# Performance work log

Measured on AMD Instinct MI355X. Metric: run time of the kernel, lower is better.

## Reference

```python
import jax, jax.numpy as jnp
import numpy as np
import math

STRIDES = (8, 16, 32, 64, 128)
IMAGE_SIZE = 1024
NUM_CLASSES = 81
B, N = 8, 64


def _calc_level_thresholds(strides, image_size):
    result = []
    last_size = image_size
    for i in range(len(strides) - 1, -1, -1):
        s = strides[i]
        pixel_size = float(s) / image_size
        th_max = math.ceil(last_size / s)
        if th_max % 2:
            th_max += 1
        th_min = th_max // 2
        last_size = th_min * s
        if i == 0:
            th_min = 1
        result.append((th_min * pixel_size, th_max * pixel_size))
    return tuple(result[::-1])


LEVEL_TH = _calc_level_thresholds(STRIDES, IMAGE_SIZE)


def setup_inputs():
    key = jax.random.key(0)
    kb, kl = jax.random.split(key)
    # normalized xyxy boxes with x1<x2, y1<y2
    xy = jax.random.uniform(kb, (B, N, 2, 2), dtype=jnp.float32)
    mins = jnp.min(xy, axis=2)
    maxs = jnp.clip(jnp.max(xy, axis=2) + 0.01, 0.0, 1.0)
    boxes = jnp.concatenate([mins, maxs], axis=-1)  # (B, N, 4)
    labels = jax.random.randint(kl, (B, N), 1, NUM_CLASSES)  # foreground classes (0 = background)
    return {"boxes": boxes, "labels": labels}


def _map_level(boxes, labels, stride, th):
    # boxes sorted by descending area along axis 1, so the LAST matching box
    Bn, Nn = boxes.shape[:2]
    H = IMAGE_SIZE // stride
    ps = stride / IMAGE_SIZE
    coords = (jnp.arange(H, dtype=boxes.dtype) + 0.5) * ps  # normalized cell centers
    mx = coords[None, None, None, :]  # varies along W
    my = coords[None, None, :, None]  # varies along H
    x1 = boxes[..., 0][:, :, None, None]
    y1 = boxes[..., 1][:, :, None, None]
    x2 = boxes[..., 2][:, :, None, None]
    y2 = boxes[..., 3][:, :, None, None]
    l = mx - x1
    t = my - y1
    r = x2 - mx
    b = y2 - my  # (B, N, H, W)
    mn = jnp.minimum(jnp.minimum(l, t), jnp.minimum(r, b))
    mxv = jnp.maximum(jnp.maximum(l, t), jnp.maximum(r, b))
    fg = mn >= 0                                   # inside-box mask (_filter_background)
    pred = fg & (mxv > th[0]) & (mxv <= th[1])     # level fit (_pointwise_fit_in_level)
    box_idx = jnp.arange(Nn)[None, :, None, None]
    win = jnp.max(jnp.where(pred, box_idx, -1), axis=1)
    has_win = win >= 0
    winc = jnp.maximum(win, 0)
    bidx = jnp.arange(Bn)[:, None, None]
    bw = boxes[bidx, winc]   # (B, H, W, 4) winning box per cell
    lw = labels[bidx, winc]  # (B, H, W)
    gx = coords[None, None, :]
    gy = coords[None, :, None]
    lL = gx - bw[..., 0]
    tT = gy - bw[..., 1]
    rR = bw[..., 2] - gx
    bB = bw[..., 3] - gy
    reg = jnp.where(has_win[..., None], jnp.stack([lL, tT, rR, bB], axis=-1), 0.0)
    dx = jnp.minimum(lL, rR)
    Dx = jnp.maximum(lL, rR)
    dy = jnp.minimum(tT, bB)
    Dy = jnp.maximum(tT, bB)
    arg = (dx / jnp.where(Dx != 0, Dx, 1.0)) * (dy / jnp.where(Dy != 0, Dy, 1.0))
    cent = jnp.where(has_win & (arg > 0), jnp.sqrt(jnp.where(arg > 0, arg, 1.0)), 0.0)
    # class map: winner one-hot; otherwise background channel 1 unless any box covers the cell
    fg_any = jnp.any(fg, axis=1)  # (B, H, W) -- _clear_box_background accumulated effect
    onehot = jax.nn.one_hot(lw, NUM_CLASSES, dtype=boxes.dtype)
    bg = jnp.zeros_like(onehot).at[..., 0].set(jnp.where(fg_any, 0.0, 1.0))
    cls = jnp.where(has_win[..., None], onehot, bg)
    level_map = jnp.concatenate([reg, cent[..., None], cls], axis=-1)  # (B, H, W, 5+C)
    return jnp.transpose(level_map, (0, 3, 1, 2))  # (B, 5+C, H, W)


def _forward(boxes, labels):
    area = (boxes[..., 2] - boxes[..., 0]) * (boxes[..., 3] - boxes[..., 1])
    order = jnp.argsort(-area, axis=1)  # descending area, as in sorted(..., reverse=True)
    boxes_s = jnp.take_along_axis(boxes, order[..., None], axis=1)
    labels_s = jnp.take_along_axis(labels, order, axis=1)
    return tuple(_map_level(boxes_s, labels_s, s, th) for s, th in zip(STRIDES, LEVEL_TH))


def reference(boxes, labels):
    return _forward(boxes, labels)
```

## Files before the change

kernel.cpp:

```cpp
#include <hip/hip_runtime.h>

#define NBATCH 8
#define NBOX   64
#define NCLS   81
#define NCH    86


__global__ __launch_bounds__(64) void fcos_mapper(
    const float* __restrict__ boxes,
    const int*   __restrict__ labels,
    float*       __restrict__ out)
{
    const int tid = threadIdx.x;
    const int bid = blockIdx.x;

    int rel, logH; float ps, tlo, thi; int base0;
    if (bid < 2048)      { rel = bid;        logH = 7; ps = 0.0078125f; tlo = 0.0078125f; thi = 0.0625f; base0 = 0; }
    else if (bid < 2560) { rel = bid - 2048; logH = 6; ps = 0.015625f;  tlo = 0.0625f;    thi = 0.125f;  base0 = 11272192; }
    else if (bid < 2688) { rel = bid - 2560; logH = 5; ps = 0.03125f;   tlo = 0.125f;     thi = 0.25f;   base0 = 14090240; }
    else if (bid < 2720) { rel = bid - 2688; logH = 4; ps = 0.0625f;    tlo = 0.25f;      thi = 0.5f;    base0 = 14794752; }
    else                 { rel = bid - 2720; logH = 3; ps = 0.125f;     tlo = 0.5f;       thi = 1.0f;    base0 = 14970880; }

    const int H      = 1 << logH;
    const int HW     = 1 << (2 * logH);
    const int logbpb = 2 * logH - 6;
    const int b      = rel >> logbpb;
    const int chunk  = rel & ((1 << logbpb) - 1);
    const int cell   = (chunk << 6) + tid;
    const int y      = cell >> logH;
    const int x      = cell & (H - 1);

    __shared__ float4 sbx[NBOX];
    __shared__ float  sa[NBOX];
    __shared__ int    sl[NBOX];
    {
        const float4 bx = reinterpret_cast<const float4*>(boxes)[b * NBOX + tid];
        const float area = (bx.z - bx.x) * (bx.w - bx.y);
        sa[tid] = area;
        __syncthreads();
        int rank = 0;
        #pragma unroll
        for (int j = 0; j < NBOX; ++j) {
            const float aj = sa[j];
            rank += ((aj > area) || (aj == area && j < tid)) ? 1 : 0;
        }
        sbx[rank] = bx;
        sl[rank]  = labels[b * NBOX + tid];
        __syncthreads();
    }

    const float gx = ((float)x + 0.5f) * ps;
    const float gy = ((float)y + 0.5f) * ps;

    int  win    = -1;
    bool fg_any = false;
    #pragma unroll 8
    for (int n = 0; n < NBOX; ++n) {
        const float4 bb = sbx[n];
        const float l = gx - bb.x;
        const float t = gy - bb.y;
        const float r = bb.z - gx;
        const float d = bb.w - gy;
        const float mn = fminf(fminf(l, t), fminf(r, d));
        const float mx = fmaxf(fmaxf(l, t), fmaxf(r, d));
        const bool fg = (mn >= 0.0f);
        fg_any = fg_any || fg;
        if (fg && (mx > tlo) && (mx <= thi)) win = n;
    }

    float reg0 = 0.f, reg1 = 0.f, reg2 = 0.f, reg3 = 0.f, cent = 0.f;
    int target;
    if (win >= 0) {
        const float4 wb = sbx[win];
        const float lL = gx - wb.x;
        const float tT = gy - wb.y;
        const float rR = wb.z - gx;
        const float bB = wb.w - gy;
        reg0 = lL; reg1 = tT; reg2 = rR; reg3 = bB;
        const float dx = fminf(lL, rR), Dx = fmaxf(lL, rR);
        const float dy = fminf(tT, bB), Dy = fmaxf(tT, bB);
        const float arg = (dx / (Dx != 0.f ? Dx : 1.f)) * (dy / (Dy != 0.f ? Dy : 1.f));
        if (arg > 0.f) cent = sqrtf(arg);
        target = sl[win];
    } else {
        target = fg_any ? -1 : 0;
    }

    float* po = out + (size_t)base0 + (size_t)b * NCH * HW + cell;
    po[0]                 = reg0;
    po[(size_t)HW]        = reg1;
    po[(size_t)2 * HW]    = reg2;
    po[(size_t)3 * HW]    = reg3;
    po[(size_t)4 * HW]    = cent;
    #pragma unroll
    for (int c = 0; c < NCLS; ++c)
        po[(size_t)(5 + c) * HW] = (c == target) ? 1.0f : 0.0f;
}

extern "C" void kernel_launch(void* const* d_in, const int* in_sizes, int n_in,
                              void* d_out, int out_size, void* d_ws, size_t ws_size,
                              hipStream_t stream) {
    const float* boxes  = (const float*)d_in[0];
    const int*   labels = (const int*)d_in[1];
    float*       out    = (float*)d_out;
    fcos_mapper<<<2728, 64, 0, stream>>>(boxes, labels, out);
}
```

Measured before the change: 79.20 us.

## Process two cells per thread with 256-thread blocks and float2 stores

Each block now has 256 threads and sorts the boxes of all 8 batches into shared memory. Each thread handles two horizontally adjacent cells, sharing the y-dependent min/max work between them. Outputs are written as float2 stores, and the one-hot class map is zero-filled before the target entry is set. The grid shrinks from 2728 to 341 blocks. This cuts the number of redundant per-block sorts and the store instruction count, but lowers total thread parallelism and adds the 8-batch sort cost to every block.

```diff
diff --git a/kernel.cpp b/kernel.cpp
--- a/kernel.cpp
+++ b/kernel.cpp
@@ -1,12 +1,11 @@
 #include <hip/hip_runtime.h>
 
-#define NBATCH 8
-#define NBOX   64
-#define NCLS   81
-#define NCH    86
+#define NBOX 64
+#define NCLS 81
+#define NCH  86
 
 
-__global__ __launch_bounds__(64) void fcos_mapper(
+__global__ __launch_bounds__(256) void fcos_mapper(
     const float* __restrict__ boxes,
     const int*   __restrict__ labels,
     float*       __restrict__ out)
@@ -14,87 +13,115 @@
     const int tid = threadIdx.x;
     const int bid = blockIdx.x;
 
-    int rel, logH; float ps, tlo, thi; int base0;
-    if (bid < 2048)      { rel = bid;        logH = 7; ps = 0.0078125f; tlo = 0.0078125f; thi = 0.0625f; base0 = 0; }
-    else if (bid < 2560) { rel = bid - 2048; logH = 6; ps = 0.015625f;  tlo = 0.0625f;    thi = 0.125f;  base0 = 11272192; }
-    else if (bid < 2688) { rel = bid - 2560; logH = 5; ps = 0.03125f;   tlo = 0.125f;     thi = 0.25f;   base0 = 14090240; }
-    else if (bid < 2720) { rel = bid - 2688; logH = 4; ps = 0.0625f;    tlo = 0.25f;      thi = 0.5f;    base0 = 14794752; }
-    else                 { rel = bid - 2720; logH = 3; ps = 0.125f;     tlo = 0.5f;       thi = 1.0f;    base0 = 14970880; }
+    __shared__ float4 sbx[8][NBOX];
+    __shared__ int    sl [8][NBOX];
+    __shared__ float  sa [4][NBOX];
 
-    const int H      = 1 << logH;
-    const int HW     = 1 << (2 * logH);
-    const int logbpb = 2 * logH - 6;
-    const int b      = rel >> logbpb;
-    const int chunk  = rel & ((1 << logbpb) - 1);
-    const int cell   = (chunk << 6) + tid;
-    const int y      = cell >> logH;
-    const int x      = cell & (H - 1);
-
-    __shared__ float4 sbx[NBOX];
-    __shared__ float  sa[NBOX];
-    __shared__ int    sl[NBOX];
     {
-        const float4 bx = reinterpret_cast<const float4*>(boxes)[b * NBOX + tid];
-        const float area = (bx.z - bx.x) * (bx.w - bx.y);
-        sa[tid] = area;
-        __syncthreads();
-        int rank = 0;
+        const int slot = tid >> 6;
+        const int box  = tid & 63;
         #pragma unroll
-        for (int j = 0; j < NBOX; ++j) {
-            const float aj = sa[j];
-            rank += ((aj > area) || (aj == area && j < tid)) ? 1 : 0;
+        for (int pass = 0; pass < 2; ++pass) {
+            const int bb = pass * 4 + slot;
+            const float4 bx = reinterpret_cast<const float4*>(boxes)[bb * NBOX + box];
+            const float area = (bx.z - bx.x) * (bx.w - bx.y);
+            sa[slot][box] = area;
+            __syncthreads();
+            int rank = 0;
+            for (int j = 0; j < NBOX; ++j) {
+                const float aj = sa[slot][j];
+                rank += ((aj > area) || (aj == area && j < box)) ? 1 : 0;
+            }
+            sbx[bb][rank] = bx;
+            sl [bb][rank] = labels[bb * NBOX + box];
+            __syncthreads();
         }
-        sbx[rank] = bx;
-        sl[rank]  = labels[b * NBOX + tid];
-        __syncthreads();
     }
 
-    const float gx = ((float)x + 0.5f) * ps;
-    const float gy = ((float)y + 0.5f) * ps;
+    int rel, logH; float ps, tlo, thi; size_t base0;
+    if (bid < 256)      { rel = bid;       logH = 7; ps = 0.0078125f; tlo = 0.0078125f; thi = 0.0625f; base0 = 0; }
+    else if (bid < 320) { rel = bid - 256; logH = 6; ps = 0.015625f;  tlo = 0.0625f;    thi = 0.125f;  base0 = 11272192; }
+    else if (bid < 336) { rel = bid - 320; logH = 5; ps = 0.03125f;   tlo = 0.125f;     thi = 0.25f;   base0 = 14090240; }
+    else if (bid < 340) { rel = bid - 336; logH = 4; ps = 0.0625f;    tlo = 0.25f;      thi = 0.5f;    base0 = 14794752; }
+    else                { rel = bid - 340; logH = 3; ps = 0.125f;     tlo = 0.5f;       thi = 1.0f;    base0 = 14970880; }
 
-    int  win    = -1;
-    bool fg_any = false;
+    const int H    = 1 << logH;
+    const int HW   = 1 << (2 * logH);
+    const int lppp = 2 * logH - 1;
+    const int p    = (rel << 8) + tid;
+    const int b    = p >> lppp;
+    const int cell = (p & ((1 << lppp) - 1)) << 1;
+    const int y    = cell >> logH;
+    const int x0   = cell & (H - 1);
+
+    const float gy  = ((float)y  + 0.5f) * ps;
+    const float gx0 = ((float)x0 + 0.5f) * ps;
+    const float gx1 = gx0 + ps;
+
+    const float4* bxp = sbx[b];
+    int  win0 = -1, win1 = -1;
+    bool fga0 = false, fga1 = false;
     #pragma unroll 8
     for (int n = 0; n < NBOX; ++n) {
-        const float4 bb = sbx[n];
-        const float l = gx - bb.x;
-        const float t = gy - bb.y;
-        const float r = bb.z - gx;
-        const float d = bb.w - gy;
-        const float mn = fminf(fminf(l, t), fminf(r, d));
-        const float mx = fmaxf(fmaxf(l, t), fmaxf(r, d));
-        const bool fg = (mn >= 0.0f);
-        fg_any = fg_any || fg;
-        if (fg && (mx > tlo) && (mx <= thi)) win = n;
+        const float4 bb = bxp[n];
+        const float t    = gy - bb.y;
+        const float d    = bb.w - gy;
+        const float tbmn = fminf(t, d);
+        const float tbmx = fmaxf(t, d);
+        {
+            const float l  = gx0 - bb.x;
+            const float r  = bb.z - gx0;
+            const float mn = fminf(tbmn, fminf(l, r));
+            const float mx = fmaxf(tbmx, fmaxf(l, r));
+            const bool  fg = (mn >= 0.0f);
+            fga0 = fga0 || fg;
+            if (fg && (mx > tlo) && (mx <= thi)) win0 = n;
+        }
+        {
+            const float l  = gx1 - bb.x;
+            const float r  = bb.z - gx1;
+            const float mn = fminf(tbmn, fminf(l, r));
+            const float mx = fmaxf(tbmx, fmaxf(l, r));
+            const bool  fg = (mn >= 0.0f);
+            fga1 = fga1 || fg;
+            if (fg && (mx > tlo) && (mx <= thi)) win1 = n;
+        }
     }
 
-    float reg0 = 0.f, reg1 = 0.f, reg2 = 0.f, reg3 = 0.f, cent = 0.f;
-    int target;
-    if (win >= 0) {
-        const float4 wb = sbx[win];
-        const float lL = gx - wb.x;
-        const float tT = gy - wb.y;
-        const float rR = wb.z - gx;
-        const float bB = wb.w - gy;
-        reg0 = lL; reg1 = tT; reg2 = rR; reg3 = bB;
-        const float dx = fminf(lL, rR), Dx = fmaxf(lL, rR);
-        const float dy = fminf(tT, bB), Dy = fmaxf(tT, bB);
+    float l0=0.f, t0=0.f, r0=0.f, d0=0.f, c0=0.f;
+    float l1=0.f, t1=0.f, r1=0.f, d1=0.f, c1=0.f;
+    int tg0, tg1;
+    if (win0 >= 0) {
+        const float4 wb = bxp[win0];
+        l0 = gx0 - wb.x; t0 = gy - wb.y; r0 = wb.z - gx0; d0 = wb.w - gy;
+        const float dx = fminf(l0, r0), Dx = fmaxf(l0, r0);
+        const float dy = fminf(t0, d0), Dy = fmaxf(t0, d0);
         const float arg = (dx / (Dx != 0.f ? Dx : 1.f)) * (dy / (Dy != 0.f ? Dy : 1.f));
-        if (arg > 0.f) cent = sqrtf(arg);
-        target = sl[win];
-    } else {
-        target = fg_any ? -1 : 0;
-    }
+        c0 = (arg > 0.f) ? sqrtf(arg) : 0.f;
+        tg0 = sl[b][win0];
+    } else tg0 = fga0 ? -1 : 0;
+    if (win1 >= 0) {
+        const float4 wb = bxp[win1];
+        l1 = gx1 - wb.x; t1 = gy - wb.y; r1 = wb.z - gx1; d1 = wb.w - gy;
+        const float dx = fminf(l1, r1), Dx = fmaxf(l1, r1);
+        const float dy = fminf(t1, d1), Dy = fmaxf(t1, d1);
+        const float arg = (dx / (Dx != 0.f ? Dx : 1.f)) * (dy / (Dy != 0.f ? Dy : 1.f));
+        c1 = (arg > 0.f) ? sqrtf(arg) : 0.f;
+        tg1 = sl[b][win1];
+    } else tg1 = fga1 ? -1 : 0;
 
-    float* po = out + (size_t)base0 + (size_t)b * NCH * HW + cell;
-    po[0]                 = reg0;
-    po[(size_t)HW]        = reg1;
-    po[(size_t)2 * HW]    = reg2;
-    po[(size_t)3 * HW]    = reg3;
-    po[(size_t)4 * HW]    = cent;
+    float* po = out + base0 + (size_t)b * NCH * HW + cell;
+    *reinterpret_cast<float2*>(po + 0 * (size_t)HW) = make_float2(l0, l1);
+    *reinterpret_cast<float2*>(po + 1 * (size_t)HW) = make_float2(t0, t1);
+    *reinterpret_cast<float2*>(po + 2 * (size_t)HW) = make_float2(r0, r1);
+    *reinterpret_cast<float2*>(po + 3 * (size_t)HW) = make_float2(d0, d1);
+    *reinterpret_cast<float2*>(po + 4 * (size_t)HW) = make_float2(c0, c1);
+    const float2 z2 = make_float2(0.f, 0.f);
     #pragma unroll
     for (int c = 0; c < NCLS; ++c)
-        po[(size_t)(5 + c) * HW] = (c == target) ? 1.0f : 0.0f;
+        *reinterpret_cast<float2*>(po + (size_t)(5 + c) * HW) = z2;
+    if (tg0 >= 0) po[(size_t)(5 + tg0) * HW]     = 1.0f;
+    if (tg1 >= 0) po[(size_t)(5 + tg1) * HW + 1] = 1.0f;
 }
 
 extern "C" void kernel_launch(void* const* d_in, const int* in_sizes, int n_in,
@@ -103,5 +130,5 @@
     const float* boxes  = (const float*)d_in[0];
     const int*   labels = (const int*)d_in[1];
     float*       out    = (float*)d_out;
-    fcos_mapper<<<2728, 64, 0, stream>>>(boxes, labels, out);
+    fcos_mapper<<<341, 256, 0, stream>>>(boxes, labels, out);
 }
```

Measured after the change: 82.71 us. 4.4% more time.

## Split output into vectorized zero fill plus sparse nonzero writes

Applied to the files above, without the earlier changes.

Adds a float4 zero-fill kernel over the whole output, then a mapper kernel that writes only the regression, centerness and single one-hot entry per cell. This replaces the 86 scalar stores per cell, most of them zeros. The mapper now uses 256-thread blocks, and each block sorts the boxes of all 8 batches into shared memory. This adds a second launch and redundant per-block sorting, and the sparse stores are scattered across channel planes.

```diff
diff --git a/kernel.cpp b/kernel.cpp
--- a/kernel.cpp
+++ b/kernel.cpp
@@ -1,12 +1,19 @@
 #include <hip/hip_runtime.h>
 
-#define NBATCH 8
-#define NBOX   64
-#define NCLS   81
-#define NCH    86
+#define NBOX 64
+#define NCLS 81
+#define NCH  86
+#define OUT_ELEMS 15014912
 
 
-__global__ __launch_bounds__(64) void fcos_mapper(
+__global__ __launch_bounds__(256) void zero_fill(float4* __restrict__ out, int n4) {
+    const float4 z = make_float4(0.f, 0.f, 0.f, 0.f);
+    int i = blockIdx.x * 256 + threadIdx.x;
+    const int stride = gridDim.x * 256;
+    for (; i < n4; i += stride) out[i] = z;
+}
+
+__global__ __launch_bounds__(256) void fcos_sparse(
     const float* __restrict__ boxes,
     const int*   __restrict__ labels,
     float*       __restrict__ out)
@@ -14,49 +21,55 @@
     const int tid = threadIdx.x;
     const int bid = blockIdx.x;
 
-    int rel, logH; float ps, tlo, thi; int base0;
-    if (bid < 2048)      { rel = bid;        logH = 7; ps = 0.0078125f; tlo = 0.0078125f; thi = 0.0625f; base0 = 0; }
-    else if (bid < 2560) { rel = bid - 2048; logH = 6; ps = 0.015625f;  tlo = 0.0625f;    thi = 0.125f;  base0 = 11272192; }
-    else if (bid < 2688) { rel = bid - 2560; logH = 5; ps = 0.03125f;   tlo = 0.125f;     thi = 0.25f;   base0 = 14090240; }
-    else if (bid < 2720) { rel = bid - 2688; logH = 4; ps = 0.0625f;    tlo = 0.25f;      thi = 0.5f;    base0 = 14794752; }
-    else                 { rel = bid - 2720; logH = 3; ps = 0.125f;     tlo = 0.5f;       thi = 1.0f;    base0 = 14970880; }
+    __shared__ float4 sbx[8][NBOX];
+    __shared__ int    sl [8][NBOX];
+    __shared__ float  sa [4][NBOX];
 
-    const int H      = 1 << logH;
-    const int HW     = 1 << (2 * logH);
-    const int logbpb = 2 * logH - 6;
-    const int b      = rel >> logbpb;
-    const int chunk  = rel & ((1 << logbpb) - 1);
-    const int cell   = (chunk << 6) + tid;
-    const int y      = cell >> logH;
-    const int x      = cell & (H - 1);
+    {
+        const int slot = tid >> 6;
+        const int box  = tid & 63;
+        #pragma unroll
+        for (int pass = 0; pass < 2; ++pass) {
+            const int bb = pass * 4 + slot;
+            const float4 bx = reinterpret_cast<const float4*>(boxes)[bb * NBOX + box];
+            const float area = (bx.z - bx.x) * (bx.w - bx.y);
+            sa[slot][box] = area;
+            __syncthreads();
+            int rank = 0;
+            for (int j = 0; j < NBOX; ++j) {
+                const float aj = sa[slot][j];
+                rank += ((aj > area) || (aj == area && j < box)) ? 1 : 0;
+            }
+            sbx[bb][rank] = bx;
+            sl [bb][rank] = labels[bb * NBOX + box];
+            __syncthreads();
+        }
+    }
 
-    __shared__ float4 sbx[NBOX];
-    __shared__ float  sa[NBOX];
-    __shared__ int    sl[NBOX];
-    {
-        const float4 bx = reinterpret_cast<const float4*>(boxes)[b * NBOX + tid];
-        const float area = (bx.z - bx.x) * (bx.w - bx.y);
-        sa[tid] = area;
-        __syncthreads();
-        int rank = 0;
-        #pragma unroll
-        for (int j = 0; j < NBOX; ++j) {
-            const float aj = sa[j];
-            rank += ((aj > area) || (aj == area && j < tid)) ? 1 : 0;
-        }
-        sbx[rank] = bx;
-        sl[rank]  = labels[b * NBOX + tid];
-        __syncthreads();
-    }
+    int rel, logH; float ps, tlo, thi; size_t base0;
+    if (bid < 512)      { rel = bid;       logH = 7; ps = 0.0078125f; tlo = 0.0078125f; thi = 0.0625f; base0 = 0; }
+    else if (bid < 640) { rel = bid - 512; logH = 6; ps = 0.015625f;  tlo = 0.0625f;    thi = 0.125f;  base0 = 11272192; }
+    else if (bid < 672) { rel = bid - 640; logH = 5; ps = 0.03125f;   tlo = 0.125f;     thi = 0.25f;   base0 = 14090240; }
+    else if (bid < 680) { rel = bid - 672; logH = 4; ps = 0.0625f;    tlo = 0.25f;      thi = 0.5f;    base0 = 14794752; }
+    else                { rel = bid - 680; logH = 3; ps = 0.125f;     tlo = 0.5f;       thi = 1.0f;    base0 = 14970880; }
+
+    const int H    = 1 << logH;
+    const int HW   = 1 << (2 * logH);
+    const int p    = (rel << 8) + tid;
+    const int b    = p >> (2 * logH);
+    const int cell = p & (HW - 1);
+    const int y    = cell >> logH;
+    const int x    = cell & (H - 1);
 
     const float gx = ((float)x + 0.5f) * ps;
     const float gy = ((float)y + 0.5f) * ps;
 
+    const float4* bxp = sbx[b];
     int  win    = -1;
     bool fg_any = false;
     #pragma unroll 8
     for (int n = 0; n < NBOX; ++n) {
-        const float4 bb = sbx[n];
+        const float4 bb = bxp[n];
         const float l = gx - bb.x;
         const float t = gy - bb.y;
         const float r = bb.z - gx;
@@ -68,33 +81,27 @@
         if (fg && (mx > tlo) && (mx <= thi)) win = n;
     }
 
-    float reg0 = 0.f, reg1 = 0.f, reg2 = 0.f, reg3 = 0.f, cent = 0.f;
-    int target;
+    float* po = out + base0 + (size_t)b * NCH * HW + cell;
     if (win >= 0) {
-        const float4 wb = sbx[win];
+        const float4 wb = bxp[win];
         const float lL = gx - wb.x;
         const float tT = gy - wb.y;
         const float rR = wb.z - gx;
         const float bB = wb.w - gy;
-        reg0 = lL; reg1 = tT; reg2 = rR; reg3 = bB;
         const float dx = fminf(lL, rR), Dx = fmaxf(lL, rR);
         const float dy = fminf(tT, bB), Dy = fmaxf(tT, bB);
         const float arg = (dx / (Dx != 0.f ? Dx : 1.f)) * (dy / (Dy != 0.f ? Dy : 1.f));
-        if (arg > 0.f) cent = sqrtf(arg);
-        target = sl[win];
-    } else {
-        target = fg_any ? -1 : 0;
+        const float cent = (arg > 0.f) ? sqrtf(arg) : 0.f;
+        const int   tg   = sl[b][win];
+        po[0]              = lL;
+        po[(size_t)HW]     = tT;
+        po[(size_t)2 * HW] = rR;
+        po[(size_t)3 * HW] = bB;
+        po[(size_t)4 * HW] = cent;
+        po[(size_t)(5 + tg) * HW] = 1.0f;
+    } else if (!fg_any) {
+        po[(size_t)5 * HW] = 1.0f;
     }
-
-    float* po = out + (size_t)base0 + (size_t)b * NCH * HW + cell;
-    po[0]                 = reg0;
-    po[(size_t)HW]        = reg1;
-    po[(size_t)2 * HW]    = reg2;
-    po[(size_t)3 * HW]    = reg3;
-    po[(size_t)4 * HW]    = cent;
-    #pragma unroll
-    for (int c = 0; c < NCLS; ++c)
-        po[(size_t)(5 + c) * HW] = (c == target) ? 1.0f : 0.0f;
 }
 
 extern "C" void kernel_launch(void* const* d_in, const int* in_sizes, int n_in,
@@ -103,5 +110,6 @@
     const float* boxes  = (const float*)d_in[0];
     const int*   labels = (const int*)d_in[1];
     float*       out    = (float*)d_out;
-    fcos_mapper<<<2728, 64, 0, stream>>>(boxes, labels, out);
+    zero_fill<<<2048, 256, 0, stream>>>(reinterpret_cast<float4*>(out), OUT_ELEMS / 4);
+    fcos_sparse<<<682, 256, 0, stream>>>(boxes, labels, out);
 }
```

After: 85.96 us. 8.5% more time.
